# Performance work log

Hardware: AMD Instinct MI355X
Metric: run time of the kernel (lower is better)

The kernel has to match this reference:

```python
import jax, jax.numpy as jnp
import numpy as np

N, DH, DK, FF = 2048, 256, 64, 32


def setup_inputs() -> dict:
    key = jax.random.key(0)
    ks = jax.random.split(key, 12)
    s = lambda d: 1.0 / np.sqrt(d).astype(np.float32)
    return {
        "x": jax.random.normal(ks[0], (1, N, DH), dtype=jnp.float32),
        "adj": (jax.random.uniform(ks[1], (N, N)) < 0.05).astype(jnp.float32),
        "dense": jax.random.uniform(ks[2], (N, N), dtype=jnp.float32),
        "Wq": jax.random.normal(ks[3], (DH, DK)) * s(DH),
        "bq": jnp.zeros((DK,), jnp.float32),
        "Wk": jax.random.normal(ks[4], (DH, DK)) * s(DH),
        "bk": jnp.zeros((DK,), jnp.float32),
        "Wv": jax.random.normal(ks[5], (DH, DH)) * s(DH),
        "bv": jnp.zeros((DH,), jnp.float32),
        "W1": jax.random.normal(ks[6], (3, FF)) * s(3),
        "b1": jnp.zeros((FF,), jnp.float32),
        "W2": jax.random.normal(ks[7], (FF, FF)) * s(FF),
        "b2": jnp.zeros((FF,), jnp.float32),
        "W3": jax.random.normal(ks[8], (FF, 1)) * s(FF),
        "b3": jnp.zeros((1,), jnp.float32),
    }


def reference(x, adj, dense, Wq, bq, Wk, bk, Wv, bv, W1, b1, W2, b2, W3, b3):
    # x: (1, n, dh). Original repeats x to (n, n, dh); here we exploit that
    # q[i, j] = Q(x_j), k[i, j] = K(x_i), v[i, j] = V(x_j) so no n^2*dh tensor
    # is materialized, while the math is identical.
    x0 = x[0]                      # (n, dh)
    q = x0 @ Wq + bq               # (n, dk), Q(x_j)
    k = x0 @ Wk + bk               # (n, dk), K(x_i)
    v = x0 @ Wv + bv               # (n, dh), V(x_j)
    # out[i, j] = <Q(x_j), K(x_i)>
    scores = k @ q.T               # (n, n)
    feats = jnp.stack((scores, adj, dense), axis=2)      # (n, n, 3)
    h = jax.nn.relu(feats @ W1 + b1)                     # (n, n, FF)
    h = jax.nn.relu(h @ W2 + b2)                         # (n, n, FF)
    focus = jax.nn.softmax((h @ W3 + b3)[..., 0], axis=1)  # (n, n)
    # feature[i] = sum_j focus[i, j] * V(x_j)
    feature = focus @ v            # (n, dh)
    return feature[None]           # (1, n, dh)
```

## Files before the change

kernel.cpp:

```cpp
#include <hip/hip_runtime.h>
#include <math.h>


#define NN  2048
#define DHH 256
#define DKK 64

typedef float    f32x4 __attribute__((ext_vector_type(4)));
typedef _Float16 f16x8 __attribute__((ext_vector_type(8)));
typedef _Float16 f16x4 __attribute__((ext_vector_type(4)));
typedef _Float16 f16x2 __attribute__((ext_vector_type(2)));
typedef int      i32x2 __attribute__((ext_vector_type(2)));
typedef int      i32x4 __attribute__((ext_vector_type(4)));

#define MFMA16(a, b, c) __builtin_amdgcn_mfma_f32_16x16x16f16((a), (b), (c), 0, 0, 0)
#define MFMA32(a, b, c) __builtin_amdgcn_mfma_f32_16x16x32_f16((a), (b), (c), 0, 0, 0)

__device__ __forceinline__ int rp2(float x, float y) {
    f16x2 v = __builtin_bit_cast(f16x2, __builtin_amdgcn_cvt_pkrtz(x, y));
    const f16x2 z = {(_Float16)0, (_Float16)0};
    v = __builtin_elementwise_max(v, z);
    return __builtin_bit_cast(int, v);
}

__global__ __launch_bounds__(256) void k_qkv(
    const float* __restrict__ x,
    const float* __restrict__ Wq, const float* __restrict__ bq,
    const float* __restrict__ Wk, const float* __restrict__ bk,
    const float* __restrict__ Wv, const float* __restrict__ bv,
    _Float16* __restrict__ q16, _Float16* __restrict__ k16,
    _Float16* __restrict__ vT)
{
    __shared__ float As[32][64];
    __shared__ float Bs[32][64];
    __shared__ _Float16 Ts[64 * 72];

    const int t  = threadIdx.x;
    const int m0 = blockIdx.x * 64;
    const int yb = blockIdx.y;

    const float* W; const float* bias; int wld; int cw0;
    if (yb == 0)      { W = Wq; bias = bq; wld = 64;  cw0 = 0; }
    else if (yb == 1) { W = Wk; bias = bk; wld = 64;  cw0 = 0; }
    else              { W = Wv; bias = bv; wld = 256; cw0 = (yb - 2) * 64; }

    const int tx = t & 15, ty = t >> 4;
    float acc[4][4] = {};

    for (int k0 = 0; k0 < DHH; k0 += 32) {
        {
            const int rr = t >> 3;
            const int cc = (t & 7) * 4;
            float4 a0 = *(const float4*)(x + (size_t)(m0 + rr)      * DHH + k0 + cc);
            float4 a1 = *(const float4*)(x + (size_t)(m0 + rr + 32) * DHH + k0 + cc);
            As[cc+0][rr]    = a0.x; As[cc+1][rr]    = a0.y; As[cc+2][rr]    = a0.z; As[cc+3][rr]    = a0.w;
            As[cc+0][rr+32] = a1.x; As[cc+1][rr+32] = a1.y; As[cc+2][rr+32] = a1.z; As[cc+3][rr+32] = a1.w;
        }
        {
            const int bk_ = t >> 4;
            const int bc  = (t & 15) * 4;
            *(float4*)&Bs[bk_][bc]      = *(const float4*)(W + (size_t)(k0 + bk_)      * wld + cw0 + bc);
            *(float4*)&Bs[bk_ + 16][bc] = *(const float4*)(W + (size_t)(k0 + bk_ + 16) * wld + cw0 + bc);
        }
        __syncthreads();
        #pragma unroll
        for (int kk = 0; kk < 32; ++kk) {
            float4 a = *(const float4*)&As[kk][ty * 4];
            float4 b = *(const float4*)&Bs[kk][tx * 4];
            float av[4] = {a.x, a.y, a.z, a.w};
            float bw[4] = {b.x, b.y, b.z, b.w};
            #pragma unroll
            for (int ii = 0; ii < 4; ++ii)
                #pragma unroll
                for (int jj = 0; jj < 4; ++jj)
                    acc[ii][jj] = fmaf(av[ii], bw[jj], acc[ii][jj]);
        }
        __syncthreads();
    }

    float4 b4 = *(const float4*)&bias[cw0 + tx * 4];
    float bc4[4] = {b4.x, b4.y, b4.z, b4.w};

    if (yb < 2) {
        _Float16* outp = (yb == 0) ? q16 : k16;
        #pragma unroll
        for (int ii = 0; ii < 4; ++ii) {
            f16x4 hv;
            #pragma unroll
            for (int jj = 0; jj < 4; ++jj) hv[jj] = (_Float16)(acc[ii][jj] + bc4[jj]);
            *(f16x4*)&outp[(size_t)(m0 + ty * 4 + ii) * 64 + tx * 4] = hv;
        }
    } else {
        #pragma unroll
        for (int jj = 0; jj < 4; ++jj) {
            f16x4 hv;
            #pragma unroll
            for (int ii = 0; ii < 4; ++ii) hv[ii] = (_Float16)(acc[ii][jj] + bc4[jj]);
            *(f16x4*)&Ts[(tx * 4 + jj) * 72 + ty * 4] = hv;
        }
        __syncthreads();
        {
            const int c = t >> 2, seg = t & 3;
            f16x8 r0 = *(const f16x8*)&Ts[c * 72 + seg * 16];
            f16x8 r1 = *(const f16x8*)&Ts[c * 72 + seg * 16 + 8];
            *(f16x8*)&vT[(size_t)(cw0 + c) * NN + m0 + seg * 16]     = r0;
            *(f16x8*)&vT[(size_t)(cw0 + c) * NN + m0 + seg * 16 + 8] = r1;
        }
    }
}

__global__ __launch_bounds__(256) void k_scores(
    const _Float16* __restrict__ q16, const _Float16* __restrict__ k16,
    f16x2* __restrict__ schl)
{
    const int t    = threadIdx.x;
    const int lane = t & 63;
    const int w    = t >> 6;
    const int col  = lane & 15;
    const int q    = lane >> 4;

    const int i0 = blockIdx.y * 128 + (w >> 1) * 64;
    const int j0 = blockIdx.x * 128 + (w & 1) * 64;

    f32x4 acc[4][4] = {};

    #pragma unroll
    for (int ks = 0; ks < 2; ++ks) {
        f16x8 a[4], b[4];
        #pragma unroll
        for (int f = 0; f < 4; ++f) {
            a[f] = *(const f16x8*)&k16[(size_t)(i0 + f * 16 + col) * 64 + ks * 32 + q * 8];
            b[f] = *(const f16x8*)&q16[(size_t)(j0 + f * 16 + col) * 64 + ks * 32 + q * 8];
        }
        #pragma unroll
        for (int fm = 0; fm < 4; ++fm)
            #pragma unroll
            for (int fn = 0; fn < 4; ++fn)
                acc[fm][fn] = MFMA32(a[fm], b[fn], acc[fm][fn]);
    }

    #pragma unroll
    for (int fm = 0; fm < 4; ++fm)
        #pragma unroll
        for (int fn = 0; fn < 4; ++fn)
            #pragma unroll
            for (int r = 0; r < 4; ++r) {
                const size_t idx = (size_t)(i0 + fm * 16 + q * 4 + r) * NN + j0 + fn * 16 + col;
                const float val = acc[fm][fn][r];
                const _Float16 h = (_Float16)val;
                f16x2 pk; pk[0] = h; pk[1] = (_Float16)(val - (float)h);
                schl[idx] = pk;
            }
}

__global__ __launch_bounds__(256) void k_mlp(
    const f16x2* __restrict__ schl,
    const float* __restrict__ adj, const float* __restrict__ dense,
    const float* __restrict__ W1, const float* __restrict__ b1,
    const float* __restrict__ W2, const float* __restrict__ b2,
    const float* __restrict__ W3,
    _Float16* __restrict__ focus)
{
    __shared__ float red[8];

    const int t    = threadIdx.x;
    const int lane = t & 63;
    const int w    = t >> 6;
    const int col  = lane & 15;
    const int q    = lane >> 4;
    const int i    = blockIdx.x;

    f16x4 l1A0 = {}, l1A1 = {};
    {
        const float w0a = W1[col], w0b = W1[col + 16];
        const _Float16 h0a = (_Float16)w0a, h0b = (_Float16)w0b;
        if (q == 0) {
            l1A0[0] = h0a; l1A0[1] = h0a;
            l1A0[2] = (_Float16)W1[32 + col];
            l1A0[3] = (_Float16)W1[64 + col];
            l1A1[0] = h0b; l1A1[1] = h0b;
            l1A1[2] = (_Float16)W1[32 + col + 16];
            l1A1[3] = (_Float16)W1[64 + col + 16];
        } else if (q == 1) {
            l1A0[0] = (_Float16)(w0a - (float)h0a);
            l1A1[0] = (_Float16)(w0b - (float)h0b);
        }
    }

    f16x4 w2A[2][2];
    #pragma unroll
    for (int fh = 0; fh < 2; ++fh)
        #pragma unroll
        for (int oh = 0; oh < 2; ++oh)
            #pragma unroll
            for (int j = 0; j < 4; ++j)
                w2A[fh][oh][j] = (_Float16)W2[(fh * 16 + q * 4 + j) * 32 + oh * 16 + col];

    f16x4 a3lo, a3hi;
    #pragma unroll
    for (int j = 0; j < 4; ++j) {
        a3lo[j] = (_Float16)W3[q * 4 + j];
        a3hi[j] = (_Float16)W3[16 + q * 4 + j];
    }

    f32x4 c1a, c1b, c2a, c2b;
    #pragma unroll
    for (int r = 0; r < 4; ++r) {
        c1a[r] = b1[q * 4 + r];
        c1b[r] = b1[16 + q * 4 + r];
        c2a[r] = b2[q * 4 + r];
        c2b[r] = b2[16 + q * 4 + r];
    }

    const f16x2* srow = schl  + (size_t)i * NN;
    const float* arow = adj   + (size_t)i * NN;
    const float* drow = dense + (size_t)i * NN;

    const f32x4 zero4 = {0.f, 0.f, 0.f, 0.f};
    float lg[8];

    for (int c = 0; c < 8; ++c) {
        const int base = w * 512 + c * 64;
        const int eb4  = base + col * 4;

        i32x4  sv = *(const i32x4*)&srow[eb4];
        float4 av = *(const float4*)&arow[eb4];
        float4 dv = *(const float4*)&drow[eb4];
        const float aa[4] = {av.x, av.y, av.z, av.w};
        const float dd[4] = {dv.x, dv.y, dv.z, dv.w};

        float lgc = 0.f;
        #pragma unroll
        for (int st = 0; st < 4; ++st) {
            const int d0 = sv[st];
            const int d1 = __builtin_bit_cast(int,
                __builtin_amdgcn_cvt_pkrtz(aa[st], dd[st]));

            const int m0 = (q == 0) ? d0 : ((q == 1) ? (d0 & 0xFFFF) : 0);
            const int m1 = (q == 0) ? d1 : 0;
            i32x2 b1v = {m0, m1};
            f16x4 B1 = __builtin_bit_cast(f16x4, b1v);

            f32x4 hpA = MFMA16(l1A0, B1, c1a);
            f32x4 hpB = MFMA16(l1A1, B1, c1b);

            i32x2 p0 = { rp2(hpA[0], hpA[1]), rp2(hpA[2], hpA[3]) };
            i32x2 p1 = { rp2(hpB[0], hpB[1]), rp2(hpB[2], hpB[3]) };
            f16x4 B2f0 = __builtin_bit_cast(f16x4, p0);
            f16x4 B2f1 = __builtin_bit_cast(f16x4, p1);

            f32x4 acc0 = MFMA16(w2A[0][0], B2f0, c2a);
            acc0 = MFMA16(w2A[1][0], B2f1, acc0);
            f32x4 acc1 = MFMA16(w2A[0][1], B2f0, c2b);
            acc1 = MFMA16(w2A[1][1], B2f1, acc1);

            i32x2 p3a = { rp2(acc0[0], acc0[1]), rp2(acc0[2], acc0[3]) };
            i32x2 p3b = { rp2(acc1[0], acc1[1]), rp2(acc1[2], acc1[3]) };
            f16x4 B3f0 = __builtin_bit_cast(f16x4, p3a);
            f16x4 B3f1 = __builtin_bit_cast(f16x4, p3b);

            f32x4 c3 = MFMA16(a3lo, B3f0, zero4);
            c3 = MFMA16(a3hi, B3f1, c3);
            lgc = (q == st) ? c3[0] : lgc;
        }
        lg[c] = lgc;
    }

    float lmax = -1e30f;
    #pragma unroll
    for (int u = 0; u < 8; ++u) lmax = fmaxf(lmax, lg[u]);
    #pragma unroll
    for (int off = 32; off > 0; off >>= 1)
        lmax = fmaxf(lmax, __shfl_xor(lmax, off, 64));
    if (lane == 0) red[w] = lmax;
    __syncthreads();
    const float rmax = fmaxf(fmaxf(red[0], red[1]), fmaxf(red[2], red[3]));

    float lsum = 0.f;
    #pragma unroll
    for (int u = 0; u < 8; ++u) { lg[u] = __expf(lg[u] - rmax); lsum += lg[u]; }
    #pragma unroll
    for (int off = 32; off > 0; off >>= 1)
        lsum += __shfl_xor(lsum, off, 64);
    if (lane == 0) red[4 + w] = lsum;
    __syncthreads();
    const float inv = 1.f / (red[4] + red[5] + red[6] + red[7]);

    _Float16* hrow = focus + (size_t)i * 2 * NN;
    const int eb = w * 512 + 4 * col + q;
    #pragma unroll
    for (int u = 0; u < 8; ++u)
        hrow[eb + u * 64] = (_Float16)(lg[u] * inv);
}

__global__ __launch_bounds__(256) void k_feat(
    const _Float16* __restrict__ focus, const _Float16* __restrict__ vT,
    float* __restrict__ out)
{
    __shared__ float rbuf[3][64][8];

    const int t    = threadIdx.x;
    const int lane = t & 63;
    const int w    = t >> 6;
    const int col  = lane & 15;
    const int q    = lane >> 4;

    const int m0 = blockIdx.y * 16;
    const int n0 = blockIdx.x * 32;

    f32x4 acc0 = {}, acc1 = {};

    const size_t arow  = (size_t)(m0 + col) * (2 * NN);
    const size_t brow0 = (size_t)(n0 + col) * NN;
    const size_t brow1 = (size_t)(n0 + 16 + col) * NN;
    const int kb = w * 512 + q * 8;

    #pragma unroll 4
    for (int k0 = 0; k0 < 512; k0 += 32) {
        const int ko = kb + k0;
        f16x8 a  = *(const f16x8*)&focus[arow + ko];
        f16x8 b0 = *(const f16x8*)&vT[brow0 + ko];
        f16x8 b1 = *(const f16x8*)&vT[brow1 + ko];
        acc0 = MFMA32(a, b0, acc0);
        acc1 = MFMA32(a, b1, acc1);
    }

    if (w != 0) {
        *(float4*)&rbuf[w - 1][lane][0] = *(float4*)&acc0;
        *(float4*)&rbuf[w - 1][lane][4] = *(float4*)&acc1;
    }
    __syncthreads();

    if (w == 0) {
        #pragma unroll
        for (int j = 0; j < 3; ++j) {
            float4 p0 = *(const float4*)&rbuf[j][lane][0];
            float4 p1 = *(const float4*)&rbuf[j][lane][4];
            acc0[0] += p0.x; acc0[1] += p0.y; acc0[2] += p0.z; acc0[3] += p0.w;
            acc1[0] += p1.x; acc1[1] += p1.y; acc1[2] += p1.z; acc1[3] += p1.w;
        }
        #pragma unroll
        for (int r = 0; r < 4; ++r) {
            out[(size_t)(m0 + q * 4 + r) * DHH + n0 + col]      = acc0[r];
            out[(size_t)(m0 + q * 4 + r) * DHH + n0 + 16 + col] = acc1[r];
        }
    }
}

extern "C" void kernel_launch(void* const* d_in, const int* in_sizes, int n_in,
                              void* d_out, int out_size, void* d_ws, size_t ws_size,
                              hipStream_t stream) {
    const float* x     = (const float*)d_in[0];
    const float* adj   = (const float*)d_in[1];
    const float* dense = (const float*)d_in[2];
    const float* Wq    = (const float*)d_in[3];
    const float* bq    = (const float*)d_in[4];
    const float* Wk    = (const float*)d_in[5];
    const float* bk    = (const float*)d_in[6];
    const float* Wv    = (const float*)d_in[7];
    const float* bv    = (const float*)d_in[8];
    const float* W1    = (const float*)d_in[9];
    const float* b1    = (const float*)d_in[10];
    const float* W2    = (const float*)d_in[11];
    const float* b2    = (const float*)d_in[12];
    const float* W3    = (const float*)d_in[13];
    float* out = (float*)d_out;

    char* wsb = (char*)d_ws;
    _Float16* q16   = (_Float16*)(wsb);
    _Float16* k16   = (_Float16*)(wsb + 262144);
    _Float16* vT    = (_Float16*)(wsb + 524288);
    f16x2*    schl  = (f16x2*)   (wsb + 1572864);
    _Float16* focus = (_Float16*)(wsb + 1572864);

    hipLaunchKernelGGL(k_qkv,    dim3(32, 6),  dim3(256), 0, stream,
                       x, Wq, bq, Wk, bk, Wv, bv, q16, k16, vT);
    hipLaunchKernelGGL(k_scores, dim3(16, 16), dim3(256), 0, stream, q16, k16, schl);
    hipLaunchKernelGGL(k_mlp,    dim3(2048),   dim3(256), 0, stream,
                       schl, adj, dense, W1, b1, W2, b2, W3, focus);
    hipLaunchKernelGGL(k_feat,   dim3(8, 128), dim3(256), 0, stream,
                       focus, vT, out);
}
```

Measured before the change: 171.7 us.

## Use 16x16x32 MFMA with even/odd feature interleave in the per-edge MLP

The per-edge MLP in k_mlp switches from 16x16x16 f16 MFMAs to 16x16x32 f16 MFMAs. Hidden features are split into even and odd output rows, so the fp32 results pack straight into the next layer's 8-wide K operand with no reshuffle. Layer 1 packs score hi/lo, adj and dense into one K=32 operand, and layers 2 and 3 need fewer MFMA instructions (5 instead of 8 per step). This cuts matrix-instruction count and issue overhead in the compute-bound MLP loop, at the cost of reorganizing the weight register layouts, which must stay consistent with the MFMA operand mapping.

```diff
diff --git a/kernel.cpp b/kernel.cpp
--- a/kernel.cpp
+++ b/kernel.cpp
@@ -13,7 +13,6 @@
 typedef int      i32x2 __attribute__((ext_vector_type(2)));
 typedef int      i32x4 __attribute__((ext_vector_type(4)));
 
-#define MFMA16(a, b, c) __builtin_amdgcn_mfma_f32_16x16x16f16((a), (b), (c), 0, 0, 0)
 #define MFMA32(a, b, c) __builtin_amdgcn_mfma_f32_16x16x32_f16((a), (b), (c), 0, 0, 0)
 
 __device__ __forceinline__ int rp2(float x, float y) {
@@ -170,46 +169,40 @@
     const int q    = lane >> 4;
     const int i    = blockIdx.x;
 
-    f16x4 l1A0 = {}, l1A1 = {};
+    f16x8 l1Ae = {}, l1Ao = {};
     {
-        const float w0a = W1[col], w0b = W1[col + 16];
-        const _Float16 h0a = (_Float16)w0a, h0b = (_Float16)w0b;
+        const float w0e = W1[2 * col], w0o = W1[2 * col + 1];
+        const _Float16 h0e = (_Float16)w0e, h0o = (_Float16)w0o;
         if (q == 0) {
-            l1A0[0] = h0a; l1A0[1] = h0a;
-            l1A0[2] = (_Float16)W1[32 + col];
-            l1A0[3] = (_Float16)W1[64 + col];
-            l1A1[0] = h0b; l1A1[1] = h0b;
-            l1A1[2] = (_Float16)W1[32 + col + 16];
-            l1A1[3] = (_Float16)W1[64 + col + 16];
-        } else if (q == 1) {
-            l1A0[0] = (_Float16)(w0a - (float)h0a);
-            l1A1[0] = (_Float16)(w0b - (float)h0b);
-        }
-    }
-
-    f16x4 w2A[2][2];
-    #pragma unroll
-    for (int fh = 0; fh < 2; ++fh)
-        #pragma unroll
-        for (int oh = 0; oh < 2; ++oh)
-            #pragma unroll
-            for (int j = 0; j < 4; ++j)
-                w2A[fh][oh][j] = (_Float16)W2[(fh * 16 + q * 4 + j) * 32 + oh * 16 + col];
-
-    f16x4 a3lo, a3hi;
-    #pragma unroll
-    for (int j = 0; j < 4; ++j) {
-        a3lo[j] = (_Float16)W3[q * 4 + j];
-        a3hi[j] = (_Float16)W3[16 + q * 4 + j];
-    }
-
-    f32x4 c1a, c1b, c2a, c2b;
+            l1Ae[0] = h0e; l1Ae[1] = h0e;
+            l1Ae[2] = (_Float16)W1[32 + 2 * col];
+            l1Ae[3] = (_Float16)W1[64 + 2 * col];
+            l1Ae[4] = (_Float16)(w0e - (float)h0e);
+            l1Ao[0] = h0o; l1Ao[1] = h0o;
+            l1Ao[2] = (_Float16)W1[32 + 2 * col + 1];
+            l1Ao[3] = (_Float16)W1[64 + 2 * col + 1];
+            l1Ao[4] = (_Float16)(w0o - (float)h0o);
+        }
+    }
+
+    f16x8 w2Ae, w2Ao;
+    #pragma unroll
+    for (int j = 0; j < 8; ++j) {
+        w2Ae[j] = (_Float16)W2[(q * 8 + j) * 32 + 2 * col];
+        w2Ao[j] = (_Float16)W2[(q * 8 + j) * 32 + 2 * col + 1];
+    }
+
+    f16x8 a3;
+    #pragma unroll
+    for (int j = 0; j < 8; ++j) a3[j] = (_Float16)W3[q * 8 + j];
+
+    f32x4 c1e, c1o, c2e, c2o;
     #pragma unroll
     for (int r = 0; r < 4; ++r) {
-        c1a[r] = b1[q * 4 + r];
-        c1b[r] = b1[16 + q * 4 + r];
-        c2a[r] = b2[q * 4 + r];
-        c2b[r] = b2[16 + q * 4 + r];
+        c1e[r] = b1[q * 8 + 2 * r];
+        c1o[r] = b1[q * 8 + 2 * r + 1];
+        c2e[r] = b2[q * 8 + 2 * r];
+        c2o[r] = b2[q * 8 + 2 * r + 1];
     }
 
     const f16x2* srow = schl  + (size_t)i * NN;
@@ -236,31 +229,26 @@
             const int d1 = __builtin_bit_cast(int,
                 __builtin_amdgcn_cvt_pkrtz(aa[st], dd[st]));
 
-            const int m0 = (q == 0) ? d0 : ((q == 1) ? (d0 & 0xFFFF) : 0);
-            const int m1 = (q == 0) ? d1 : 0;
-            i32x2 b1v = {m0, m1};
-            f16x4 B1 = __builtin_bit_cast(f16x4, b1v);
-
-            f32x4 hpA = MFMA16(l1A0, B1, c1a);
-            f32x4 hpB = MFMA16(l1A1, B1, c1b);
-
-            i32x2 p0 = { rp2(hpA[0], hpA[1]), rp2(hpA[2], hpA[3]) };
-            i32x2 p1 = { rp2(hpB[0], hpB[1]), rp2(hpB[2], hpB[3]) };
-            f16x4 B2f0 = __builtin_bit_cast(f16x4, p0);
-            f16x4 B2f1 = __builtin_bit_cast(f16x4, p1);
-
-            f32x4 acc0 = MFMA16(w2A[0][0], B2f0, c2a);
-            acc0 = MFMA16(w2A[1][0], B2f1, acc0);
-            f32x4 acc1 = MFMA16(w2A[0][1], B2f0, c2b);
-            acc1 = MFMA16(w2A[1][1], B2f1, acc1);
-
-            i32x2 p3a = { rp2(acc0[0], acc0[1]), rp2(acc0[2], acc0[3]) };
-            i32x2 p3b = { rp2(acc1[0], acc1[1]), rp2(acc1[2], acc1[3]) };
-            f16x4 B3f0 = __builtin_bit_cast(f16x4, p3a);
-            f16x4 B3f1 = __builtin_bit_cast(f16x4, p3b);
-
-            f32x4 c3 = MFMA16(a3lo, B3f0, zero4);
-            c3 = MFMA16(a3hi, B3f1, c3);
+            i32x4 b1v;
+            if (q == 0) { b1v[0] = d0; b1v[1] = d1; b1v[2] = d0 & 0xFFFF; b1v[3] = 0; }
+            else        { b1v[0] = 0;  b1v[1] = 0;  b1v[2] = 0;           b1v[3] = 0; }
+            f16x8 B1 = __builtin_bit_cast(f16x8, b1v);
+
+            f32x4 h1e = MFMA32(l1Ae, B1, c1e);
+            f32x4 h1o = MFMA32(l1Ao, B1, c1o);
+
+            i32x4 p2 = { rp2(h1e[0], h1o[0]), rp2(h1e[1], h1o[1]),
+                         rp2(h1e[2], h1o[2]), rp2(h1e[3], h1o[3]) };
+            f16x8 B2 = __builtin_bit_cast(f16x8, p2);
+
+            f32x4 h2e = MFMA32(w2Ae, B2, c2e);
+            f32x4 h2o = MFMA32(w2Ao, B2, c2o);
+
+            i32x4 p3 = { rp2(h2e[0], h2o[0]), rp2(h2e[1], h2o[1]),
+                         rp2(h2e[2], h2o[2]), rp2(h2e[3], h2o[3]) };
+            f16x8 B3 = __builtin_bit_cast(f16x8, p3);
+
+            f32x4 c3 = MFMA32(a3, B3, zero4);
             lgc = (q == st) ? c3[0] : lgc;
         }
         lg[c] = lgc;
```

New measurement: 172.6 us. About the same (+0.5%).
